# Kernel tuning notes

Hardware: AMD Instinct MI355X
Metric: run time of the kernel (lower is better)

The kernel has to match this reference:

```python
import jax, jax.numpy as jnp
import numpy as np

D_MODEL = 512
NUM_HEADS = 8
DEPTH = D_MODEL // NUM_HEADS


def setup_inputs() -> dict:
    key = jax.random.key(0)
    ks = jax.random.split(key, 11)
    B, S = 2, 4096
    scale = 1.0 / np.sqrt(D_MODEL)
    inp = {
        "q": jax.random.normal(ks[0], (B, S, D_MODEL), jnp.float32),
        "k": jax.random.normal(ks[1], (B, S, D_MODEL), jnp.float32),
        "v": jax.random.normal(ks[2], (B, S, D_MODEL), jnp.float32),
        "wq_w": jax.random.normal(ks[3], (D_MODEL, D_MODEL), jnp.float32) * scale,
        "wq_b": jnp.zeros((D_MODEL,), jnp.float32),
        "wk_w": jax.random.normal(ks[4], (D_MODEL, D_MODEL), jnp.float32) * scale,
        "wk_b": jnp.zeros((D_MODEL,), jnp.float32),
        "wv_w": jax.random.normal(ks[5], (D_MODEL, D_MODEL), jnp.float32) * scale,
        "wv_b": jnp.zeros((D_MODEL,), jnp.float32),
        "wo_w": jax.random.normal(ks[6], (D_MODEL, D_MODEL), jnp.float32) * scale,
        "wo_b": jnp.zeros((D_MODEL,), jnp.float32),
    }
    return inp


def _split_heads(x):
    # [B, S, D] -> [B, H, S, depth]
    B, S, _ = x.shape
    return x.reshape(B, S, NUM_HEADS, DEPTH).transpose(0, 2, 1, 3)


def reference(q, k, v, wq_w, wq_b, wk_w, wk_b, wv_w, wv_b, wo_w, wo_b):
    B, S, _ = q.shape
    qh = _split_heads(q @ wq_w.T + wq_b)  # [B,H,S,d]
    kh = _split_heads(k @ wk_w.T + wk_b)
    vh = _split_heads(v @ wv_w.T + wv_b)
    logits = jnp.einsum('bhqd,bhkd->bhqk', qh, kh) / jnp.sqrt(
        jnp.asarray(DEPTH, jnp.float32))
    attn = jax.nn.softmax(logits, axis=-1)
    out = jnp.einsum('bhqk,bhkd->bhqd', attn, vh)  # [B,H,S,d]
    out = out.transpose(0, 2, 1, 3).reshape(B, S, D_MODEL)
    return out @ wo_w.T + wo_b
```

## Files before the change

kernel.cpp:

```cpp
#include <hip/hip_runtime.h>

typedef __attribute__((ext_vector_type(8))) short short8;
typedef __attribute__((ext_vector_type(4))) float float4v;

#define D_MODEL 512
#define NUM_HEADS 8
#define DEPTH 64
#define SEQ 4096
#define BATCH 2
#define MROWS 8192
#define SCALE_Q 0.18033688011112043f

#define SW(r, c) (((r) * 64) + ((((c) ^ ((r) & 7))) * 8))
#define SW128(n, c) (((n) * 128) + ((((c) ^ ((n) & 15))) * 8))

static __device__ __forceinline__ unsigned short f2bf(float f) {
  unsigned int u = __builtin_bit_cast(unsigned int, f);
  u += 0x7FFFu + ((u >> 16) & 1u);
  return (unsigned short)(u >> 16);
}
static __device__ __forceinline__ unsigned int pk2(float a, float b) {
  return (unsigned int)f2bf(a) | ((unsigned int)f2bf(b) << 16);
}
static __device__ __forceinline__ unsigned int pk2f(float a, float b) {
  unsigned int ua = __builtin_bit_cast(unsigned int, a) + 0x8000u;
  unsigned int ub = __builtin_bit_cast(unsigned int, b) + 0x8000u;
  return __builtin_amdgcn_perm(ub, ua, 0x07060302u);
}
static __device__ __forceinline__ short8 cvt8(const float* p) {
  float4v f0 = *(const float4v*)p;
  float4v f1 = *(const float4v*)(p + 4);
  short8 s;
#pragma unroll
  for (int j = 0; j < 4; ++j) {
    s[j] = (short)f2bf(f0[j]);
    s[4 + j] = (short)f2bf(f1[j]);
  }
  return s;
}

struct QkvA {
  const float* X[3];
  const float* W[3];
  const float* bias[3];
  unsigned short* out[3];
};
__global__ __launch_bounds__(256) void gemm128_qkv(QkvA a) {
  __shared__ unsigned short smem[2 * 128 * 64];
  unsigned short* As = smem;
  unsigned short* Bs = smem + 128 * 64;
  const int z = blockIdx.z;
  const float* __restrict__ X = a.X[z];
  const float* __restrict__ W = a.W[z];
  const float* __restrict__ bias = a.bias[z];
  unsigned short* __restrict__ out = a.out[z];
  const int t = threadIdx.x;
  const int w = t >> 6, l = t & 63, lq = l >> 4, lm = l & 15;
  const int mq = (w & 1) * 64, nq = (w >> 1) * 64;
  const int mBase = blockIdx.x * 128, nBase = blockIdx.y * 128;
  float4v acc[4][4] = {};
  for (int kc = 0; kc < D_MODEL; kc += 64) {
    __syncthreads();
#pragma unroll
    for (int p = 0; p < 4; ++p) {
      int i = p * 256 + t, r = i >> 3, c = i & 7;
      *(short8*)&As[SW(r, c)] = cvt8(&X[(size_t)(mBase + r) * D_MODEL + kc + c * 8]);
      *(short8*)&Bs[SW(r, c)] = cvt8(&W[(size_t)(nBase + r) * D_MODEL + kc + c * 8]);
    }
    __syncthreads();
#pragma unroll
    for (int kk = 0; kk < 2; ++kk) {
      short8 av[4];
#pragma unroll
      for (int fm = 0; fm < 4; ++fm)
        av[fm] = *(const short8*)&As[SW(mq + fm * 16 + lm, kk * 4 + lq)];
#pragma unroll
      for (int fn = 0; fn < 4; ++fn) {
        short8 bv = *(const short8*)&Bs[SW(nq + fn * 16 + lm, kk * 4 + lq)];
#pragma unroll
        for (int fm = 0; fm < 4; ++fm)
          acc[fm][fn] = __builtin_amdgcn_mfma_f32_16x16x32_bf16(av[fm], bv, acc[fm][fn], 0, 0, 0);
      }
    }
  }
  if (z == 2) {
    __syncthreads();
    unsigned short* T = smem;
#pragma unroll
    for (int fn = 0; fn < 4; ++fn) {
      int n = nq + fn * 16 + lm;
      float bv = bias[nBase + n];
#pragma unroll
      for (int fm = 0; fm < 4; ++fm) {
        int m0 = mq + fm * 16 + lq * 4;
        uint2 u;
        u.x = pk2(acc[fm][fn][0] + bv, acc[fm][fn][1] + bv);
        u.y = pk2(acc[fm][fn][2] + bv, acc[fm][fn][3] + bv);
        *(uint2*)&T[SW128(n, m0 >> 3) + (lq & 1) * 4] = u;
      }
    }
    __syncthreads();
    const int bb = mBase >> 12, s0 = mBase & 4095;
#pragma unroll
    for (int p = 0; p < 8; ++p) {
      int i = p * 256 + t, n = i >> 4, cm = i & 15;
      int gn = nBase + n, h = gn >> 6, d = gn & 63;
      *(short8*)&out[(((size_t)(bb * NUM_HEADS + h) * DEPTH + d) << 12) + s0 + cm * 8] =
          *(const short8*)&T[SW128(n, cm)];
    }
  } else {
    const float scale = (z == 0) ? SCALE_Q : 1.0f;
#pragma unroll
    for (int fn = 0; fn < 4; ++fn) {
      int gn = nBase + nq + fn * 16 + lm;
      float bv = bias[gn];
      int h = gn >> 6, d = gn & 63;
#pragma unroll
      for (int fm = 0; fm < 4; ++fm) {
#pragma unroll
        for (int r = 0; r < 4; ++r) {
          int gm = mBase + mq + fm * 16 + lq * 4 + r;
          int bb = gm >> 12, s = gm & 4095;
          out[(((size_t)(bb * NUM_HEADS + h) * SEQ + s) << 6) + d] =
              f2bf((acc[fm][fn][r] + bv) * scale);
        }
      }
    }
  }
}

__global__ __launch_bounds__(256) void gemm_out_128x64(
    const unsigned short* __restrict__ X,
    const float* __restrict__ W,
    const float* __restrict__ bias,
    float* __restrict__ out) {
  __shared__ unsigned short As[128 * 64];
  __shared__ unsigned short Bs[64 * 64];
  const int t = threadIdx.x;
  const int w = t >> 6, l = t & 63, lq = l >> 4, lm = l & 15;
  const int mq = w * 32;
  const int mBase = blockIdx.x * 128, nBase = blockIdx.y * 64;
  float4v acc[2][4] = {};
  for (int kc = 0; kc < D_MODEL; kc += 64) {
    __syncthreads();
#pragma unroll
    for (int p = 0; p < 4; ++p) {
      int i = p * 256 + t, r = i >> 3, c = i & 7;
      *(short8*)&As[SW(r, c)] = *(const short8*)&X[(size_t)(mBase + r) * D_MODEL + kc + c * 8];
    }
#pragma unroll
    for (int p = 0; p < 2; ++p) {
      int i = p * 256 + t, r = i >> 3, c = i & 7;
      *(short8*)&Bs[SW(r, c)] = cvt8(&W[(size_t)(nBase + r) * D_MODEL + kc + c * 8]);
    }
    __syncthreads();
#pragma unroll
    for (int kk = 0; kk < 2; ++kk) {
      short8 av[2];
#pragma unroll
      for (int fm = 0; fm < 2; ++fm)
        av[fm] = *(const short8*)&As[SW(mq + fm * 16 + lm, kk * 4 + lq)];
#pragma unroll
      for (int fn = 0; fn < 4; ++fn) {
        short8 bv = *(const short8*)&Bs[SW(fn * 16 + lm, kk * 4 + lq)];
#pragma unroll
        for (int fm = 0; fm < 2; ++fm)
          acc[fm][fn] = __builtin_amdgcn_mfma_f32_16x16x32_bf16(av[fm], bv, acc[fm][fn], 0, 0, 0);
      }
    }
  }
#pragma unroll
  for (int fn = 0; fn < 4; ++fn) {
    int gn = nBase + fn * 16 + lm;
    float bv = bias[gn];
#pragma unroll
    for (int fm = 0; fm < 2; ++fm) {
#pragma unroll
      for (int r = 0; r < 4; ++r) {
        int gm = mBase + mq + fm * 16 + lq * 4 + r;
        out[(size_t)gm * D_MODEL + gn] = acc[fm][fn][r] + bv;
      }
    }
  }
}

__global__ __launch_bounds__(256) void attn(
    const unsigned short* __restrict__ Qh,
    const unsigned short* __restrict__ Kh,
    const unsigned short* __restrict__ Vt,
    unsigned short* __restrict__ AO)
{
  __shared__ unsigned short Ksub[2][64 * 64];
  __shared__ unsigned short Vsub[2][64 * 64];
  __shared__ unsigned short Psub[128 * 64];
  const int t = threadIdx.x;
  const int w = t >> 6;
  const int l = t & 63, lq = l >> 4, lm = l & 15;
  const int bh = blockIdx.y;
  const size_t base = (size_t)bh * SEQ * DEPTH;
  const int qbase = blockIdx.x * 128 + w * 32;
  const unsigned short* __restrict__ Kp = Kh + base;
  const unsigned short* __restrict__ Vp = Vt + base;

  short8 qf[2][2];
#pragma unroll
  for (int qb = 0; qb < 2; ++qb)
#pragma unroll
    for (int kk = 0; kk < 2; ++kk)
      qf[qb][kk] = *(const short8*)&Qh[base + (size_t)(qbase + qb * 16 + lm) * DEPTH + kk * 32 + lq * 8];

  short8 ones;
#pragma unroll
  for (int j = 0; j < 8; ++j) ones[j] = (short)0x3F80;

  float4v oacc[2][4] = {};
  float4v sumacc[2] = {};
  short8 kreg[2], vreg[2];

#pragma unroll
  for (int p = 0; p < 2; ++p) {
    int i = p * 256 + t, r = i >> 3, c = i & 7;
    kreg[p] = *(const short8*)&Kp[(size_t)r * DEPTH + c * 8];
    vreg[p] = *(const short8*)&Vp[(size_t)r * SEQ + c * 8];
  }
#pragma unroll
  for (int p = 0; p < 2; ++p) {
    int i = p * 256 + t, r = i >> 3, c = i & 7;
    *(short8*)&Ksub[0][SW(r, c)] = kreg[p];
    *(short8*)&Vsub[0][SW(r, c)] = vreg[p];
  }
  __syncthreads();

  auto step = [&](int cur, int tile, bool pf) {
    if (pf) {
      const int s0n = (tile + 1) * 64;
#pragma unroll
      for (int p = 0; p < 2; ++p) {
        int i = p * 256 + t, r = i >> 3, c = i & 7;
        kreg[p] = *(const short8*)&Kp[(size_t)(s0n + r) * DEPTH + c * 8];
        vreg[p] = *(const short8*)&Vp[(size_t)r * SEQ + s0n + c * 8];
      }
    }
#pragma unroll
    for (int f = 0; f < 4; ++f) {
      float4v sacc[2] = {};
#pragma unroll
      for (int kk = 0; kk < 2; ++kk) {
        short8 a = *(const short8*)&Ksub[cur][SW(f * 16 + lm, kk * 4 + lq)];
        sacc[0] = __builtin_amdgcn_mfma_f32_16x16x32_bf16(a, qf[0][kk], sacc[0], 0, 0, 0);
        sacc[1] = __builtin_amdgcn_mfma_f32_16x16x32_bf16(a, qf[1][kk], sacc[1], 0, 0, 0);
      }
#pragma unroll
      for (int qb = 0; qb < 2; ++qb) {
        uint2 u;
        u.x = pk2f(__builtin_amdgcn_exp2f(sacc[qb][0]), __builtin_amdgcn_exp2f(sacc[qb][1]));
        u.y = pk2f(__builtin_amdgcn_exp2f(sacc[qb][2]), __builtin_amdgcn_exp2f(sacc[qb][3]));
        *(uint2*)&Psub[SW(w * 32 + qb * 16 + lm, 2 * f + (lq >> 1)) + (lq & 1) * 4] = u;
      }
    }
#pragma unroll
    for (int kk = 0; kk < 2; ++kk) {
      short8 a0 = *(const short8*)&Psub[SW(w * 32 + lm, kk * 4 + lq)];
      short8 a1 = *(const short8*)&Psub[SW(w * 32 + 16 + lm, kk * 4 + lq)];
      sumacc[0] = __builtin_amdgcn_mfma_f32_16x16x32_bf16(a0, ones, sumacc[0], 0, 0, 0);
      sumacc[1] = __builtin_amdgcn_mfma_f32_16x16x32_bf16(a1, ones, sumacc[1], 0, 0, 0);
#pragma unroll
      for (int df = 0; df < 4; ++df) {
        short8 b = *(const short8*)&Vsub[cur][SW(df * 16 + lm, kk * 4 + lq)];
        oacc[0][df] = __builtin_amdgcn_mfma_f32_16x16x32_bf16(a0, b, oacc[0][df], 0, 0, 0);
        oacc[1][df] = __builtin_amdgcn_mfma_f32_16x16x32_bf16(a1, b, oacc[1][df], 0, 0, 0);
      }
    }
    if (pf) {
#pragma unroll
      for (int p = 0; p < 2; ++p) {
        int i = p * 256 + t, r = i >> 3, c = i & 7;
        *(short8*)&Ksub[cur ^ 1][SW(r, c)] = kreg[p];
        *(short8*)&Vsub[cur ^ 1][SW(r, c)] = vreg[p];
      }
    }
    __syncthreads();
  };

  for (int it = 0; it < 64; it += 2) {
    step(0, it, true);
    step(1, it + 1, it + 2 < 64);
  }

  const int bb = bh >> 3, h = bh & 7;
#pragma unroll
  for (int qb = 0; qb < 2; ++qb) {
#pragma unroll
    for (int r = 0; r < 4; ++r) {
      float rinv = 1.0f / sumacc[qb][r];
      int s = qbase + qb * 16 + lq * 4 + r;
#pragma unroll
      for (int df = 0; df < 4; ++df) {
        int d = df * 16 + lm;
        AO[((size_t)(bb * SEQ + s)) * D_MODEL + h * DEPTH + d] = f2bf(oacc[qb][df][r] * rinv);
      }
    }
  }
}

extern "C" void kernel_launch(void* const* d_in, const int* in_sizes, int n_in,
                              void* d_out, int out_size, void* d_ws, size_t ws_size,
                              hipStream_t stream) {
  const float* q = (const float*)d_in[0];
  const float* k = (const float*)d_in[1];
  const float* v = (const float*)d_in[2];
  const float* wq = (const float*)d_in[3];
  const float* bq = (const float*)d_in[4];
  const float* wk = (const float*)d_in[5];
  const float* bk = (const float*)d_in[6];
  const float* wv = (const float*)d_in[7];
  const float* bv = (const float*)d_in[8];
  const float* wo = (const float*)d_in[9];
  const float* bo = (const float*)d_in[10];

  const size_t HSD = (size_t)BATCH * NUM_HEADS * SEQ * DEPTH;
  unsigned short* ws = (unsigned short*)d_ws;
  unsigned short* Qh = ws;
  unsigned short* Kh = Qh + HSD;
  unsigned short* Vt = Kh + HSD;
  unsigned short* AO = Vt + HSD;

  QkvA qa;
  qa.X[0] = q; qa.X[1] = k; qa.X[2] = v;
  qa.W[0] = wq; qa.W[1] = wk; qa.W[2] = wv;
  qa.bias[0] = bq; qa.bias[1] = bk; qa.bias[2] = bv;
  qa.out[0] = Qh; qa.out[1] = Kh; qa.out[2] = Vt;
  gemm128_qkv<<<dim3(MROWS / 128, D_MODEL / 128, 3), 256, 0, stream>>>(qa);

  attn<<<dim3(SEQ / 128, BATCH * NUM_HEADS), 256, 0, stream>>>(Qh, Kh, Vt, AO);

  gemm_out_128x64<<<dim3(MROWS / 128, D_MODEL / 64), 256, 0, stream>>>(AO, wo, bo, (float*)d_out);
}
```

Measured before the change: 274.7 us.

## Pre-convert weights to bf16 and compute full-N QKV tiles per block

Adds small kernels that convert the projection weights to bf16 once per call, reusing spare workspace regions. The QKV GEMM is restructured so each block computes a 64-row by full 512-column tile, so every X tile is read and converted only once instead of four times. Weights now come from bf16 staging with no per-tile conversion. The output GEMM also reads pre-converted bf16 weights. The cost is two extra launches and a large 64KB shared-memory weight tile per block, which may limit occupancy.

```diff
diff --git a/kernel.cpp b/kernel.cpp
--- a/kernel.cpp
+++ b/kernel.cpp
@@ -9,10 +9,10 @@
 #define SEQ 4096
 #define BATCH 2
 #define MROWS 8192
+#define WSZ (D_MODEL * D_MODEL)
 #define SCALE_Q 0.18033688011112043f
 
 #define SW(r, c) (((r) * 64) + ((((c) ^ ((r) & 7))) * 8))
-#define SW128(n, c) (((n) * 128) + ((((c) ^ ((n) & 15))) * 8))
 
 static __device__ __forceinline__ unsigned short f2bf(float f) {
   unsigned int u = __builtin_bit_cast(unsigned int, f);
@@ -39,33 +39,55 @@
   return s;
 }
 
-struct QkvA {
+__global__ __launch_bounds__(256) void cvt3(const float* __restrict__ w0,
+                                            const float* __restrict__ w1,
+                                            const float* __restrict__ w2,
+                                            unsigned short* __restrict__ dst) {
+  const float* srcs[3] = {w0, w1, w2};
+  const int z = blockIdx.y;
+  const float4v* s = (const float4v*)srcs[z];
+  uint2* d = (uint2*)(dst + (size_t)z * WSZ);
+  int i = blockIdx.x * 256 + threadIdx.x;
+  float4v f = s[i];
+  d[i] = make_uint2(pk2(f[0], f[1]), pk2(f[2], f[3]));
+}
+__global__ __launch_bounds__(256) void cvt1(const float* __restrict__ w,
+                                            unsigned short* __restrict__ dst) {
+  int i = blockIdx.x * 256 + threadIdx.x;
+  float4v f = ((const float4v*)w)[i];
+  ((uint2*)dst)[i] = make_uint2(pk2(f[0], f[1]), pk2(f[2], f[3]));
+}
+
+struct QkvB {
   const float* X[3];
-  const float* W[3];
   const float* bias[3];
   unsigned short* out[3];
 };
-__global__ __launch_bounds__(256) void gemm128_qkv(QkvA a) {
-  __shared__ unsigned short smem[2 * 128 * 64];
-  unsigned short* As = smem;
-  unsigned short* Bs = smem + 128 * 64;
-  const int z = blockIdx.z;
+__global__ __launch_bounds__(256, 2) void qkv_fulln(QkvB a,
+                                                    const unsigned short* __restrict__ Wall) {
+  __shared__ unsigned short Xs[64 * 64];
+  __shared__ unsigned short Ws[512 * 64];
+  const int z = blockIdx.y;
   const float* __restrict__ X = a.X[z];
-  const float* __restrict__ W = a.W[z];
+  const unsigned short* __restrict__ W = Wall + (size_t)z * WSZ;
   const float* __restrict__ bias = a.bias[z];
   unsigned short* __restrict__ out = a.out[z];
   const int t = threadIdx.x;
   const int w = t >> 6, l = t & 63, lq = l >> 4, lm = l & 15;
-  const int mq = (w & 1) * 64, nq = (w >> 1) * 64;
-  const int mBase = blockIdx.x * 128, nBase = blockIdx.y * 128;
-  float4v acc[4][4] = {};
+  const int mBase = blockIdx.x * 64;
+  float4v acc[4][8] = {};
+
   for (int kc = 0; kc < D_MODEL; kc += 64) {
     __syncthreads();
 #pragma unroll
-    for (int p = 0; p < 4; ++p) {
+    for (int p = 0; p < 2; ++p) {
       int i = p * 256 + t, r = i >> 3, c = i & 7;
-      *(short8*)&As[SW(r, c)] = cvt8(&X[(size_t)(mBase + r) * D_MODEL + kc + c * 8]);
-      *(short8*)&Bs[SW(r, c)] = cvt8(&W[(size_t)(nBase + r) * D_MODEL + kc + c * 8]);
+      *(short8*)&Xs[SW(r, c)] = cvt8(&X[(size_t)(mBase + r) * D_MODEL + kc + c * 8]);
+    }
+#pragma unroll 4
+    for (int p = 0; p < 16; ++p) {
+      int i = p * 256 + t, r = i >> 3, c = i & 7;
+      *(short8*)&Ws[SW(r, c)] = *(const short8*)&W[(size_t)r * D_MODEL + kc + c * 8];
     }
     __syncthreads();
 #pragma unroll
@@ -73,54 +95,53 @@
       short8 av[4];
 #pragma unroll
       for (int fm = 0; fm < 4; ++fm)
-        av[fm] = *(const short8*)&As[SW(mq + fm * 16 + lm, kk * 4 + lq)];
-#pragma unroll
-      for (int fn = 0; fn < 4; ++fn) {
-        short8 bv = *(const short8*)&Bs[SW(nq + fn * 16 + lm, kk * 4 + lq)];
+        av[fm] = *(const short8*)&Xs[SW(fm * 16 + lm, kk * 4 + lq)];
+#pragma unroll
+      for (int fn = 0; fn < 8; ++fn) {
+        short8 bv = *(const short8*)&Ws[SW(w * 128 + fn * 16 + lm, kk * 4 + lq)];
 #pragma unroll
         for (int fm = 0; fm < 4; ++fm)
           acc[fm][fn] = __builtin_amdgcn_mfma_f32_16x16x32_bf16(av[fm], bv, acc[fm][fn], 0, 0, 0);
       }
     }
   }
+  const int bb = mBase >> 12, s0 = mBase & 4095;
   if (z == 2) {
     __syncthreads();
-    unsigned short* T = smem;
-#pragma unroll
-    for (int fn = 0; fn < 4; ++fn) {
-      int n = nq + fn * 16 + lm;
-      float bv = bias[nBase + n];
+    unsigned short* T = Ws;
+#pragma unroll
+    for (int fn = 0; fn < 8; ++fn) {
+      int n = w * 128 + fn * 16 + lm;
+      float bv = bias[n];
 #pragma unroll
       for (int fm = 0; fm < 4; ++fm) {
-        int m0 = mq + fm * 16 + lq * 4;
+        int m0 = fm * 16 + lq * 4;
         uint2 u;
         u.x = pk2(acc[fm][fn][0] + bv, acc[fm][fn][1] + bv);
         u.y = pk2(acc[fm][fn][2] + bv, acc[fm][fn][3] + bv);
-        *(uint2*)&T[SW128(n, m0 >> 3) + (lq & 1) * 4] = u;
-      }
-    }
-    __syncthreads();
-    const int bb = mBase >> 12, s0 = mBase & 4095;
-#pragma unroll
-    for (int p = 0; p < 8; ++p) {
-      int i = p * 256 + t, n = i >> 4, cm = i & 15;
-      int gn = nBase + n, h = gn >> 6, d = gn & 63;
+        *(uint2*)&T[SW(n, m0 >> 3) + (lq & 1) * 4] = u;
+      }
+    }
+    __syncthreads();
+#pragma unroll
+    for (int p = 0; p < 16; ++p) {
+      int i = p * 256 + t, n = i >> 3, cm = i & 7;
+      int h = n >> 6, d = n & 63;
       *(short8*)&out[(((size_t)(bb * NUM_HEADS + h) * DEPTH + d) << 12) + s0 + cm * 8] =
-          *(const short8*)&T[SW128(n, cm)];
+          *(const short8*)&T[SW(n, cm)];
     }
   } else {
     const float scale = (z == 0) ? SCALE_Q : 1.0f;
 #pragma unroll
-    for (int fn = 0; fn < 4; ++fn) {
-      int gn = nBase + nq + fn * 16 + lm;
+    for (int fn = 0; fn < 8; ++fn) {
+      int gn = w * 128 + fn * 16 + lm;
       float bv = bias[gn];
       int h = gn >> 6, d = gn & 63;
 #pragma unroll
       for (int fm = 0; fm < 4; ++fm) {
 #pragma unroll
         for (int r = 0; r < 4; ++r) {
-          int gm = mBase + mq + fm * 16 + lq * 4 + r;
-          int bb = gm >> 12, s = gm & 4095;
+          int s = s0 + fm * 16 + lq * 4 + r;
           out[(((size_t)(bb * NUM_HEADS + h) * SEQ + s) << 6) + d] =
               f2bf((acc[fm][fn][r] + bv) * scale);
         }
@@ -131,7 +152,7 @@
 
 __global__ __launch_bounds__(256) void gemm_out_128x64(
     const unsigned short* __restrict__ X,
-    const float* __restrict__ W,
+    const unsigned short* __restrict__ W,
     const float* __restrict__ bias,
     float* __restrict__ out) {
   __shared__ unsigned short As[128 * 64];
@@ -151,7 +172,7 @@
 #pragma unroll
     for (int p = 0; p < 2; ++p) {
       int i = p * 256 + t, r = i >> 3, c = i & 7;
-      *(short8*)&Bs[SW(r, c)] = cvt8(&W[(size_t)(nBase + r) * D_MODEL + kc + c * 8]);
+      *(short8*)&Bs[SW(r, c)] = *(const short8*)&W[(size_t)(nBase + r) * D_MODEL + kc + c * 8];
     }
     __syncthreads();
 #pragma unroll
@@ -324,15 +345,20 @@
   unsigned short* Kh = Qh + HSD;
   unsigned short* Vt = Kh + HSD;
   unsigned short* AO = Vt + HSD;
-
-  QkvA qa;
+  unsigned short* Wqkv = AO;
+  unsigned short* Wo = Vt;
+
+  cvt3<<<dim3(WSZ / 4 / 256, 3), 256, 0, stream>>>(wq, wk, wv, Wqkv);
+
+  QkvB qa;
   qa.X[0] = q; qa.X[1] = k; qa.X[2] = v;
-  qa.W[0] = wq; qa.W[1] = wk; qa.W[2] = wv;
   qa.bias[0] = bq; qa.bias[1] = bk; qa.bias[2] = bv;
   qa.out[0] = Qh; qa.out[1] = Kh; qa.out[2] = Vt;
-  gemm128_qkv<<<dim3(MROWS / 128, D_MODEL / 128, 3), 256, 0, stream>>>(qa);
+  qkv_fulln<<<dim3(MROWS / 64, 3), 256, 0, stream>>>(qa, Wqkv);
 
   attn<<<dim3(SEQ / 128, BATCH * NUM_HEADS), 256, 0, stream>>>(Qh, Kh, Vt, AO);
 
-  gemm_out_128x64<<<dim3(MROWS / 128, D_MODEL / 64), 256, 0, stream>>>(AO, wo, bo, (float*)d_out);
-}
+  cvt1<<<WSZ / 4 / 256, 256, 0, stream>>>(wo, Wo);
+
+  gemm_out_128x64<<<dim3(MROWS / 128, D_MODEL / 64), 256, 0, stream>>>(AO, Wo, bo, (float*)d_out);
+}
```

New measurement: 235.5 us. 1.17x faster.
